# Optimization experiments

Measured on AMD Instinct MI355X. Metric: run time of the kernel, lower is better.

## Reference

```python
import jax, jax.numpy as jnp
import numpy as np

B = 524288
H = 20          # heads
NUM_EX = 13     # embedding rows
EMB = 3         # embedding dim
FEAT_IN, FEAT_OUT = 3, 5
HEAD_IN, HEAD_HID = 8, 10


def setup_inputs() -> dict:
    key = jax.random.key(0)
    ks = jax.random.split(key, 12)
    e = jax.random.randint(ks[0], (B, H), 0, NUM_EX)
    f = jax.random.normal(ks[1], (B, H * FEAT_IN), dtype=jnp.float32)
    # embedding table; row 0 zeroed as in the torch __init__
    emb = jax.random.normal(ks[2], (NUM_EX, EMB), dtype=jnp.float32) * 0.1
    emb = emb.at[0].set(0.0)
    # features Linear(3 -> 5), stored as (in, out) so y = x @ Wf + bf
    Wf = jax.random.normal(ks[3], (FEAT_IN, FEAT_OUT), dtype=jnp.float32) * 0.5
    bf = jax.random.normal(ks[4], (FEAT_OUT,), dtype=jnp.float32) * 0.1
    # 20 parallel head MLPs, batched over the head axis
    W1 = jax.random.normal(ks[5], (H, HEAD_IN, HEAD_HID), dtype=jnp.float32) * 0.3
    b1 = jax.random.normal(ks[6], (H, HEAD_HID), dtype=jnp.float32) * 0.1
    W2 = jax.random.normal(ks[7], (H, HEAD_HID), dtype=jnp.float32) * 0.3
    b2 = jax.random.normal(ks[8], (H,), dtype=jnp.float32) * 0.1
    # output Linear(20 -> 1)
    Wo = jax.random.normal(ks[9], (H, 1), dtype=jnp.float32) * 0.3
    bo = jax.random.normal(ks[10], (1,), dtype=jnp.float32) * 0.1
    return {"e": e, "f": f, "emb": emb, "Wf": Wf, "bf": bf,
            "W1": W1, "b1": b1, "W2": W2, "b2": b2, "Wo": Wo, "bo": bo}


def reference(e, f, emb, Wf, bf, W1, b1, W2, b2, Wo, bo):
    ev = emb[e]                                    # (B, 20, 3) embedding lookup
    fv = f.reshape(-1, H, FEAT_IN) @ Wf + bf       # (B, 20, 5)
    x = jnp.concatenate([ev, fv], axis=2)          # (B, 20, 8)
    # all 20 heads as one batched matmul instead of a Python loop
    h1 = jax.nn.leaky_relu(jnp.einsum('bhi,hio->bho', x, W1) + b1)  # (B, 20, 10)
    h = jax.nn.softplus(jnp.einsum('bho,ho->bh', h1, W2) + b2)      # (B, 20)
    return h @ Wo + bo                             # (B, 1)
```

## Files before the change

kernel.cpp:

```cpp
#include <hip/hip_runtime.h>


#define HH   20
#define NEX  13

__device__ __forceinline__ float softplus_fast(float x) {
    return fmaxf(x, 0.0f) + __logf(1.0f + __expf(-fabsf(x)));
}

template<int J>
__device__ __forceinline__ float head_group(
    int4 iv, float4 fa, float4 fb, float4 fc,
    const float4* __restrict__ s_emb,
    const float* __restrict__ Wf, const float* __restrict__ bf,
    const float* __restrict__ W1, const float* __restrict__ b1,
    const float* __restrict__ W2, const float* __restrict__ b2,
    const float* __restrict__ Wo)
{
    int   ii[4]  = { iv.x, iv.y, iv.z, iv.w };
    float ff[12] = { fa.x, fa.y, fa.z, fa.w,
                     fb.x, fb.y, fb.z, fb.w,
                     fc.x, fc.y, fc.z, fc.w };
    float partial = 0.0f;

#pragma unroll
    for (int t = 0; t < 4; ++t) {
        const int h = 4 * J + t;
        float4 ev = s_emb[ii[t]];

        float xv[8];
        xv[0] = ev.x; xv[1] = ev.y; xv[2] = ev.z;

        float g0 = ff[3 * t + 0], g1 = ff[3 * t + 1], g2 = ff[3 * t + 2];
#pragma unroll
        for (int o = 0; o < 5; ++o) {
            float a = bf[o];
            a = fmaf(g0, Wf[0 * 5 + o], a);
            a = fmaf(g1, Wf[1 * 5 + o], a);
            a = fmaf(g2, Wf[2 * 5 + o], a);
            xv[3 + o] = a;
        }

        float hacc = b2[h];
#pragma unroll
        for (int o = 0; o < 10; ++o) {
            float a = b1[h * 10 + o];
#pragma unroll
            for (int k = 0; k < 8; ++k)
                a = fmaf(xv[k], W1[(h * 8 + k) * 10 + o], a);
            a = fmaxf(a, 0.01f * a);
            hacc = fmaf(a, W2[h * 10 + o], hacc);
        }

        partial = fmaf(softplus_fast(hacc), Wo[h], partial);
    }
    return partial;
}

__global__ __launch_bounds__(320, 6) void airfit_kernel(
    const int*   __restrict__ e,   const float* __restrict__ f,
    const float* __restrict__ emb, const float* __restrict__ Wf,
    const float* __restrict__ bf,  const float* __restrict__ W1,
    const float* __restrict__ b1,  const float* __restrict__ W2,
    const float* __restrict__ b2,  const float* __restrict__ Wo,
    const float* __restrict__ bo,  float* __restrict__ out, int B)
{
    __shared__ float4 s_emb[NEX];
    __shared__ float  s_part[5][64];

    if (threadIdx.x < NEX) {
        int r = threadIdx.x;
        s_emb[r] = make_float4(emb[3 * r + 0], emb[3 * r + 1],
                               emb[3 * r + 2], 0.0f);
    }
    __syncthreads();

    const int i    = threadIdx.x & 63;
    const int jj   = threadIdx.x >> 6;
    const int item = blockIdx.x * 64 + i;

    if (item < B) {
        int4 iv = *(reinterpret_cast<const int4*>(e + (size_t)item * HH) + jj);
        const float4* fp =
            reinterpret_cast<const float4*>(f + (size_t)item * (HH * 3)) + 3 * jj;
        float4 fa = fp[0], fb = fp[1], fc = fp[2];

        const int j = __builtin_amdgcn_readfirstlane(jj);
        float partial;
        switch (j) {
        case 0:  partial = head_group<0>(iv, fa, fb, fc, s_emb, Wf, bf, W1, b1, W2, b2, Wo); break;
        case 1:  partial = head_group<1>(iv, fa, fb, fc, s_emb, Wf, bf, W1, b1, W2, b2, Wo); break;
        case 2:  partial = head_group<2>(iv, fa, fb, fc, s_emb, Wf, bf, W1, b1, W2, b2, Wo); break;
        case 3:  partial = head_group<3>(iv, fa, fb, fc, s_emb, Wf, bf, W1, b1, W2, b2, Wo); break;
        default: partial = head_group<4>(iv, fa, fb, fc, s_emb, Wf, bf, W1, b1, W2, b2, Wo); break;
        }
        s_part[jj][i] = partial;
    }
    __syncthreads();

    if (jj == 0 && item < B) {
        float r = bo[0] + s_part[0][i] + s_part[1][i] + s_part[2][i]
                        + s_part[3][i] + s_part[4][i];
        out[item] = r;
    }
}

extern "C" void kernel_launch(void* const* d_in, const int* in_sizes, int n_in,
                              void* d_out, int out_size, void* d_ws, size_t ws_size,
                              hipStream_t stream) {
    const int*   e   = (const int*)  d_in[0];
    const float* f   = (const float*)d_in[1];
    const float* emb = (const float*)d_in[2];
    const float* Wf  = (const float*)d_in[3];
    const float* bf  = (const float*)d_in[4];
    const float* W1  = (const float*)d_in[5];
    const float* b1  = (const float*)d_in[6];
    const float* W2  = (const float*)d_in[7];
    const float* b2  = (const float*)d_in[8];
    const float* Wo  = (const float*)d_in[9];
    const float* bo  = (const float*)d_in[10];
    float* out = (float*)d_out;

    int B = in_sizes[0] / HH;
    int blocks = (B + 63) / 64;
    airfit_kernel<<<blocks, 320, 0, stream>>>(e, f, emb, Wf, bf, W1, b1,
                                              W2, b2, Wo, bo, out, B);
}
```

Baseline: 269.3 us.

## Fold embedding and feature linear into precomputed per-head tables

A setup kernel precomputes, per head, the product of the feature Linear weights with W1 (a 3x10 matrix M), plus a table holding embedding@W1 + bf@W1 + b1 for every embedding index. The main kernel then does one table lookup plus 3 FMAs per hidden unit instead of 8 FMAs plus the feature linear. This removes most of the per-item first-layer arithmetic. The cost is an extra kernel launch, about 12 KB of shared memory per block filled from the workspace on every block, and wider LDS row reads that may bank-conflict and lower occupancy.

```diff
diff --git a/kernel.cpp b/kernel.cpp
--- a/kernel.cpp
+++ b/kernel.cpp
@@ -3,17 +3,45 @@
 
 #define HH   20
 #define NEX  13
+#define TST  12
+#define WS_M 0
+#define WS_T 640
 
 __device__ __forceinline__ float softplus_fast(float x) {
     return fmaxf(x, 0.0f) + __logf(1.0f + __expf(-fabsf(x)));
 }
 
+__global__ void airfit_setup(const float* __restrict__ emb,
+                             const float* __restrict__ Wf,
+                             const float* __restrict__ bf,
+                             const float* __restrict__ W1,
+                             const float* __restrict__ b1,
+                             float* __restrict__ ws)
+{
+    int t = blockIdx.x * 256 + threadIdx.x;
+    if (t < HH * 3 * 10) {
+        int h = t / 30, c = (t / 10) % 3, o = t % 10;
+        float a = 0.0f;
+        for (int q = 0; q < 5; ++q)
+            a += Wf[c * 5 + q] * W1[(h * 8 + 3 + q) * 10 + o];
+        ws[WS_M + (h * 3 + c) * 10 + o] = a;
+    }
+    if (t < HH * NEX * 10) {
+        int h = t / (NEX * 10), idx = (t / 10) % NEX, o = t % 10;
+        float a = b1[h * 10 + o];
+        for (int i = 0; i < 3; ++i)
+            a += emb[idx * 3 + i] * W1[(h * 8 + i) * 10 + o];
+        for (int q = 0; q < 5; ++q)
+            a += bf[q] * W1[(h * 8 + 3 + q) * 10 + o];
+        ws[WS_T + (h * NEX + idx) * TST + o] = a;
+    }
+}
+
 template<int J>
 __device__ __forceinline__ float head_group(
     int4 iv, float4 fa, float4 fb, float4 fc,
-    const float4* __restrict__ s_emb,
-    const float* __restrict__ Wf, const float* __restrict__ bf,
-    const float* __restrict__ W1, const float* __restrict__ b1,
+    const float* __restrict__ s_T,
+    const float* __restrict__ M,
     const float* __restrict__ W2, const float* __restrict__ b2,
     const float* __restrict__ Wo)
 {
@@ -26,32 +54,24 @@
 #pragma unroll
     for (int t = 0; t < 4; ++t) {
         const int h = 4 * J + t;
-        float4 ev = s_emb[ii[t]];
-
-        float xv[8];
-        xv[0] = ev.x; xv[1] = ev.y; xv[2] = ev.z;
+        const float* Trow = s_T + (h * NEX + ii[t]) * TST;
+        float4 t0 = *reinterpret_cast<const float4*>(Trow);
+        float4 t1 = *reinterpret_cast<const float4*>(Trow + 4);
+        float2 t2 = *reinterpret_cast<const float2*>(Trow + 8);
+        float pre[10] = { t0.x, t0.y, t0.z, t0.w,
+                          t1.x, t1.y, t1.z, t1.w, t2.x, t2.y };
 
         float g0 = ff[3 * t + 0], g1 = ff[3 * t + 1], g2 = ff[3 * t + 2];
-#pragma unroll
-        for (int o = 0; o < 5; ++o) {
-            float a = bf[o];
-            a = fmaf(g0, Wf[0 * 5 + o], a);
-            a = fmaf(g1, Wf[1 * 5 + o], a);
-            a = fmaf(g2, Wf[2 * 5 + o], a);
-            xv[3 + o] = a;
-        }
-
         float hacc = b2[h];
 #pragma unroll
         for (int o = 0; o < 10; ++o) {
-            float a = b1[h * 10 + o];
-#pragma unroll
-            for (int k = 0; k < 8; ++k)
-                a = fmaf(xv[k], W1[(h * 8 + k) * 10 + o], a);
+            float a = pre[o];
+            a = fmaf(g0, M[(h * 3 + 0) * 10 + o], a);
+            a = fmaf(g1, M[(h * 3 + 1) * 10 + o], a);
+            a = fmaf(g2, M[(h * 3 + 2) * 10 + o], a);
             a = fmaxf(a, 0.01f * a);
             hacc = fmaf(a, W2[h * 10 + o], hacc);
         }
-
         partial = fmaf(softplus_fast(hacc), Wo[h], partial);
     }
     return partial;
@@ -59,25 +79,21 @@
 
 __global__ __launch_bounds__(320, 6) void airfit_kernel(
     const int*   __restrict__ e,   const float* __restrict__ f,
-    const float* __restrict__ emb, const float* __restrict__ Wf,
-    const float* __restrict__ bf,  const float* __restrict__ W1,
-    const float* __restrict__ b1,  const float* __restrict__ W2,
+    const float* __restrict__ ws,  const float* __restrict__ W2,
     const float* __restrict__ b2,  const float* __restrict__ Wo,
     const float* __restrict__ bo,  float* __restrict__ out, int B)
 {
-    __shared__ float4 s_emb[NEX];
-    __shared__ float  s_part[5][64];
+    __shared__ float s_T[HH * NEX * TST];
+    __shared__ float s_part[5][64];
 
-    if (threadIdx.x < NEX) {
-        int r = threadIdx.x;
-        s_emb[r] = make_float4(emb[3 * r + 0], emb[3 * r + 1],
-                               emb[3 * r + 2], 0.0f);
-    }
+    for (int t = threadIdx.x; t < HH * NEX * TST; t += 320)
+        s_T[t] = ws[WS_T + t];
     __syncthreads();
 
     const int i    = threadIdx.x & 63;
     const int jj   = threadIdx.x >> 6;
     const int item = blockIdx.x * 64 + i;
+    const float* M = ws + WS_M;
 
     if (item < B) {
         int4 iv = *(reinterpret_cast<const int4*>(e + (size_t)item * HH) + jj);
@@ -88,11 +104,11 @@
         const int j = __builtin_amdgcn_readfirstlane(jj);
         float partial;
         switch (j) {
-        case 0:  partial = head_group<0>(iv, fa, fb, fc, s_emb, Wf, bf, W1, b1, W2, b2, Wo); break;
-        case 1:  partial = head_group<1>(iv, fa, fb, fc, s_emb, Wf, bf, W1, b1, W2, b2, Wo); break;
-        case 2:  partial = head_group<2>(iv, fa, fb, fc, s_emb, Wf, bf, W1, b1, W2, b2, Wo); break;
-        case 3:  partial = head_group<3>(iv, fa, fb, fc, s_emb, Wf, bf, W1, b1, W2, b2, Wo); break;
-        default: partial = head_group<4>(iv, fa, fb, fc, s_emb, Wf, bf, W1, b1, W2, b2, Wo); break;
+        case 0:  partial = head_group<0>(iv, fa, fb, fc, s_T, M, W2, b2, Wo); break;
+        case 1:  partial = head_group<1>(iv, fa, fb, fc, s_T, M, W2, b2, Wo); break;
+        case 2:  partial = head_group<2>(iv, fa, fb, fc, s_T, M, W2, b2, Wo); break;
+        case 3:  partial = head_group<3>(iv, fa, fb, fc, s_T, M, W2, b2, Wo); break;
+        default: partial = head_group<4>(iv, fa, fb, fc, s_T, M, W2, b2, Wo); break;
         }
         s_part[jj][i] = partial;
     }
@@ -120,9 +136,12 @@
     const float* Wo  = (const float*)d_in[9];
     const float* bo  = (const float*)d_in[10];
     float* out = (float*)d_out;
+    float* ws  = (float*)d_ws;
 
     int B = in_sizes[0] / HH;
+
+    airfit_setup<<<11, 256, 0, stream>>>(emb, Wf, bf, W1, b1, ws);
+
     int blocks = (B + 63) / 64;
-    airfit_kernel<<<blocks, 320, 0, stream>>>(e, f, emb, Wf, bf, W1, b1,
-                                              W2, b2, Wo, bo, out, B);
+    airfit_kernel<<<blocks, 320, 0, stream>>>(e, f, ws, W2, b2, Wo, bo, out, B);
 }
```

New measurement: 269.8 us. About the same (+0.2%).
